# Optimization experiments

Measured on AMD Instinct MI355X. Metric: run time of the kernel, lower is better.

## Reference

```python
import jax, jax.numpy as jnp
import numpy as np

N = 6144      # nodes
DIN = 65      # input_dim (1 time + 64 space coords)
DOUT = 65     # output_dim per head
H = 4         # nheads
EPS = 1e-7
MIN = 1e-15
# curvature c = 1 throughout (MultiHeadGraphAttentionLayer hardcodes curvature=1)

def arcosh(z):
    return jnp.log(z + jnp.sqrt(jnp.maximum(z * z - 1.0, 0.0)))

def hyp_proj(u):
    # project onto hyperboloid: recompute time coord
    y = u[..., 1:]
    t = jnp.sqrt(1.0 + jnp.sum(y * y, -1, keepdims=True))
    return jnp.concatenate([t, y], -1)

def expmap0(u):
    v = u[..., 1:]
    n = jnp.maximum(jnp.linalg.norm(v, axis=-1, keepdims=True), MIN)
    return jnp.concatenate([jnp.cosh(n), jnp.sinh(n) * v / n], -1)

def logmap0(x):
    y = x[..., 1:]
    n = jnp.maximum(jnp.linalg.norm(y, axis=-1, keepdims=True), MIN)
    t = jnp.maximum(x[..., :1], 1.0 + EPS)
    return jnp.concatenate([jnp.zeros_like(t), arcosh(t) * y / n], -1)

def hyp_linear(x, W):
    # HypLinear (use_bias=False, eval mode): mobius_matvec = exp0(log0(x) @ W^T), then proj
    return hyp_proj(expmap0(logmap0(x) @ W.T))

def to_poincare(x):
    return x[..., 1:] / (x[..., :1] + 1.0)

def to_hyperboloid(p):
    s = jnp.sum(p * p, -1, keepdims=True)
    return jnp.concatenate([1.0 + s, 2.0 * p], -1) / jnp.maximum(1.0 - s, MIN)

def mobius_half(v):
    # 0.5 (x) v  (mobius scalar multiplication, c=1)
    n = jnp.maximum(jnp.linalg.norm(v, axis=-1, keepdims=True), MIN)
    return jnp.tanh(0.5 * jnp.arctanh(jnp.minimum(n, 1.0 - EPS))) * v / n

def head(x, adj_t, Wa, Wd, Wo):
    att = hyp_linear(x, Wa)   # [N, DOUT]
    red = hyp_linear(x, Wd)   # [N, DOUT]
    # pairwise hyperboloid sqdist via Minkowski inner product (negate time coord)
    am = att.at[:, 0].multiply(-1.0)
    theta = jnp.maximum(-(am @ att.T), 1.0 + EPS)          # [N, N]
    S = jnp.minimum(arcosh(theta) ** 2, 50.0)
    # coef[i, j] = -adj[j, i] * sqdist for incoming edges (mask = adj^T)
    coef = jnp.where(adj_t > 0.01, -adj_t * S, 0.0)
    # F.normalize along incoming-edge axis (zeros don't change the L2 norm)
    a = coef / jnp.maximum(jnp.linalg.norm(coef, axis=-1, keepdims=True), 1e-12)
    pv = to_poincare(red)                                   # [N, DOUT-1]
    lam = 2.0 / jnp.maximum(1.0 - jnp.sum(pv * pv, -1), MIN)  # conformal factors [N]
    num = (a * lam[None, :]) @ pv                           # [N, DOUT-1]
    den = jnp.sum(jnp.abs(a) * (lam - 1.0)[None, :], -1, keepdims=True)
    m = mobius_half(num / jnp.maximum(den, MIN))            # mobius midpoint
    return hyp_linear(to_hyperboloid(m), Wo)                # [N, DOUT]

def reference(x, adj, W_att, W_data, W_out, W_lin):
    adj_t = adj.T
    hs = jnp.stack([head(x, adj_t, W_att[h], W_data[h], W_out[h]) for h in range(H)], axis=1)  # [N, H, DOUT]
    p = to_poincare(hs).reshape(x.shape[0], -1)             # PoincareBall.concat -> [N, H*(DOUT-1)]
    return hyp_linear(to_hyperboloid(p), W_lin)             # [N, H*DOUT]

def setup_inputs():
    key = jax.random.key(0)
    ks = jax.random.split(key, 8)
    sp = 0.1 * jax.random.normal(ks[0], (N, DIN - 1), jnp.float32)
    x = jnp.concatenate([jnp.sqrt(1.0 + jnp.sum(sp * sp, -1, keepdims=True)), sp], -1)
    adj = (jax.random.uniform(ks[1], (N, N)) < 32.0 / N).astype(jnp.float32)
    adj = jnp.maximum(adj, jnp.eye(N, dtype=jnp.float32))  # every node >=1 incoming edge
    def xavier(k, shape):
        b = (6.0 / (shape[0] + shape[1])) ** 0.5
        return jax.random.uniform(k, shape, jnp.float32, -b, b)
    W_att = jnp.stack([xavier(jax.random.fold_in(ks[2], h), (DOUT, DIN)) for h in range(H)])
    W_data = jnp.stack([xavier(jax.random.fold_in(ks[3], h), (DOUT, DIN)) for h in range(H)])
    W_out = jnp.stack([xavier(jax.random.fold_in(ks[4], h), (DOUT, DOUT)) for h in range(H)])
    W_lin = xavier(ks[5], (H * DOUT, H * (DOUT - 1) + 1))
    return {"x": x, "adj": adj, "W_att": W_att, "W_data": W_data, "W_out": W_out, "W_lin": W_lin}
```

## Files before the change

kernel.cpp:

```cpp
#include <hip/hip_runtime.h>
#include <math.h>

#define N 6144
#define H 4
#define CAP 128
#define MINF 1e-15f
#define ONE_EPS  1.0000001192092896f
#define ONE_MEPS 0.9999998807907104f

__device__ __forceinline__ float wave_reduce_sum(float v) {
    v += __shfl_xor(v, 32, 64);
    v += __shfl_xor(v, 16, 64);
    v += __shfl_xor(v, 8, 64);
    v += __shfl_xor(v, 4, 64);
    v += __shfl_xor(v, 2, 64);
    v += __shfl_xor(v, 1, 64);
    return v;
}

__device__ __forceinline__ float arcosh_f(float z) {
    return logf(z + sqrtf(fmaxf(z * z - 1.0f, 0.0f)));
}

__global__ void k_prep(const float* __restrict__ x, float* __restrict__ lmv,
                       const float* __restrict__ W_att, const float* __restrict__ W_data,
                       const float* __restrict__ W_out, const float* __restrict__ Wl,
                       float* __restrict__ Bp, float* __restrict__ Bo,
                       float* __restrict__ WlT, int* __restrict__ cnt) {
    int b = blockIdx.x;
    if (b < 1536) {
        int i = b * 4 + (threadIdx.x >> 6);
        int lane = threadIdx.x & 63;
        float y = x[i * 65 + 1 + lane];
        float ss = wave_reduce_sum(y * y);
        float n = fmaxf(sqrtf(ss), MINF);
        float t = fmaxf(x[i * 65], ONE_EPS);
        lmv[i * 64 + lane] = arcosh_f(t) * y / n;
    } else if (b < 1728) {
        int tid = (b - 1536) * 256 + threadIdx.x;
        int m = tid >> 12;
        int r = tid & 4095;
        int k = r >> 6, o = r & 63;
        const float* src;
        if (m < 4) src = W_att + m * 65 * 65;
        else if (m < 8) src = W_data + (m - 4) * 65 * 65;
        else src = W_out + (m - 8) * 65 * 65;
        float val = src[(1 + o) * 65 + (1 + k)];
        if (m < 8) Bp[m * 4096 + k * 64 + o] = val;
        else Bo[(m - 8) * 4096 + k * 64 + o] = val;
    } else if (b < 1808) {
        int L = ((b - 1728) * 256 + threadIdx.x) * 4;
        int k = L / 320, o0 = L % 320;
        float v[4];
        #pragma unroll
        for (int q = 0; q < 4; q++) {
            int o = o0 + q;
            v[q] = (o < 259) ? Wl[(size_t)(1 + o) * 257 + 1 + k] : 0.f;
        }
        *(float4*)(WlT + L) = make_float4(v[0], v[1], v[2], v[3]);
    } else {
        cnt[(b - 1808) * 256 + threadIdx.x] = 0;
    }
}

__global__ void __launch_bounds__(256) k_csr_gemm(
        const float* __restrict__ adj, int* __restrict__ cnt, int* __restrict__ idx,
        const float* __restrict__ lmv, const float* __restrict__ Bp,
        float* __restrict__ attv, float2* __restrict__ a0l, float* __restrict__ pv) {
    __shared__ float smem[64 * 65];
    if (blockIdx.x < 768) {
        float (*As)[64] = (float(*)[64])smem;
        float (*Bs)[64] = (float(*)[64])(smem + 1024);
        float (*Cs)[65] = (float(*)[65])smem;
        int my = blockIdx.x / 96;
        int ix = blockIdx.x % 96;
        const float* Bb = Bp + (size_t)my * 4096;
        int i0 = ix * 64;
        int tid = threadIdx.x;
        int tx = tid & 15, ty = tid >> 4;
        float acc[4][4] = {};
        for (int k0 = 0; k0 < 64; k0 += 16) {
            {
                int mm = tid >> 2, kq = tid & 3;
                float4 v = *(const float4*)(lmv + (size_t)(i0 + mm) * 64 + k0 + kq * 4);
                As[kq * 4 + 0][mm] = v.x;
                As[kq * 4 + 1][mm] = v.y;
                As[kq * 4 + 2][mm] = v.z;
                As[kq * 4 + 3][mm] = v.w;
            }
            {
                int kk = tid >> 4, o4 = tid & 15;
                float4 bvv = *(const float4*)(Bb + (k0 + kk) * 64 + o4 * 4);
                *(float4*)&Bs[kk][o4 * 4] = bvv;
            }
            __syncthreads();
            #pragma unroll
            for (int kk = 0; kk < 16; kk++) {
                float4 av = *(const float4*)&As[kk][ty * 4];
                float4 bv = *(const float4*)&Bs[kk][tx * 4];
                float a[4] = {av.x, av.y, av.z, av.w};
                float b[4] = {bv.x, bv.y, bv.z, bv.w};
                #pragma unroll
                for (int r = 0; r < 4; r++)
                    #pragma unroll
                    for (int c = 0; c < 4; c++) acc[r][c] += a[r] * b[c];
            }
            __syncthreads();
        }
        #pragma unroll
        for (int r = 0; r < 4; r++)
            #pragma unroll
            for (int c = 0; c < 4; c++)
                Cs[ty * 4 + r][tx * 4 + c] = acc[r][c];
        __syncthreads();
        int w = tid >> 6, lane = tid & 63;
        bool isAtt = my < 4;
        int h = my & 3;
        #pragma unroll 1
        for (int r = 0; r < 16; r++) {
            int row = w * 16 + r;
            int i = i0 + row;
            float u = Cs[row][lane];
            float nn = fmaxf(sqrtf(wave_reduce_sum(u * u)), MINF);
            if (isAtt) {
                float sha = sinhf(nn);
                attv[((size_t)h * N + i) * 64 + lane] = sha * u / nn;
                if (lane == 0) a0l[h * N + i].x = coshf(nn);
            } else {
                float shd = sinhf(nn), chd = coshf(nn);
                float pvd = (shd * u / nn) / (chd + 1.0f);
                pv[((size_t)h * N + i) * 64 + lane] = pvd;
                float sp = wave_reduce_sum(pvd * pvd);
                if (lane == 0) a0l[h * N + i].y = 2.0f / fmaxf(1.0f - sp, MINF);
            }
        }
    } else {
        const float4* a4 = (const float4*)adj;
        const unsigned STRIDE = 1048576u;
        unsigned e0 = (blockIdx.x - 768) * 256 + threadIdx.x;
        float4 v0 = a4[e0];
        float4 v1 = a4[e0 + STRIDE];
        #pragma unroll 1
        for (int it = 0; it < 9; it++) {
            float4 vn;
            if (it < 7) vn = a4[e0 + (unsigned)(it + 2) * STRIDE];
            unsigned base = (e0 + (unsigned)it * STRIDE) * 4u;
            float vals[4] = {v0.x, v0.y, v0.z, v0.w};
            #pragma unroll
            for (int q = 0; q < 4; q++) {
                if (vals[q] > 0.01f) {
                    unsigned t = base + q;
                    int j = t / N;
                    int i = t % N;
                    int pos = atomicAdd(&cnt[i], 1);
                    if (pos < CAP) idx[i * CAP + pos] = j;
                }
            }
            v0 = v1;
            v1 = vn;
        }
    }
}

__global__ void __launch_bounds__(256) k_attn(
        const int* __restrict__ cnt, const int* __restrict__ idx,
        const float* __restrict__ attv, const float2* __restrict__ a0l,
        const float* __restrict__ pv, float* __restrict__ lm2) {
    __shared__ float wls[4][CAP];
    __shared__ int jls[4][CAP];
    int w = threadIdx.x >> 6, lane = threadIdx.x & 63;
    int i = blockIdx.x * 4 + w;
    int h = blockIdx.y;
    const float* attvh = attv + (size_t)h * N * 64;
    const float* pvh = pv + (size_t)h * N * 64;
    const float2* a0lh = a0l + (size_t)h * N;

    int c = lane & 3;
    float4 aireg[4];
    #pragma unroll
    for (int q = 0; q < 4; q++)
        aireg[q] = *(const float4*)(attvh + (size_t)i * 64 + q * 16 + c * 4);
    float ai0 = a0lh[i].x;
    int nn = min(cnt[i], CAP);

    float accd = 0.f, accss = 0.f;
    for (int base = 0; base < nn; base += 16) {
        int t = base + (lane >> 2);
        bool act = t < nn;
        int j = act ? idx[i * CAP + t] : i;
        float2 al = a0lh[j];
        float d = 0.f;
        #pragma unroll
        for (int q = 0; q < 4; q++) {
            float4 b = *(const float4*)(attvh + (size_t)j * 64 + q * 16 + c * 4);
            float4 a = aireg[q];
            d += a.x * b.x + a.y * b.y + a.z * b.z + a.w * b.w;
        }
        d += __shfl_xor(d, 1, 64);
        d += __shfl_xor(d, 2, 64);
        float theta = fmaxf(ai0 * al.x - d, ONE_EPS);
        float ar = arcosh_f(theta);
        float S = fminf(ar * ar, 50.0f);
        if (!act) S = 0.f;
        if (c == 0) {
            accd += S * (al.y - 1.0f);
            accss += S * S;
            wls[w][t] = S * al.y;
            jls[w][t] = j;
        }
    }
    accd = wave_reduce_sum(accd);
    accss = wave_reduce_sum(accss);
    float nrm = fmaxf(sqrtf(accss), 1e-12f);
    float den = fmaxf(accd / nrm, MINF);
    float scl = 1.0f / (nrm * den);

    float accn = 0.f;
    #pragma unroll 4
    for (int t = 0; t < nn; t++) {
        int j = jls[w][t];
        float wq = wls[w][t];
        accn = fmaf(wq, pvh[(size_t)j * 64 + lane], accn);
    }
    float v = -scl * accn;
    float nv = fmaxf(sqrtf(wave_reduce_sum(v * v)), MINF);
    float nc = fminf(nv, ONE_MEPS);
    float mh = tanhf(0.5f * atanhf(nc));
    float md = mh * v / nv;
    float s = wave_reduce_sum(md * md);
    float Dh = fmaxf(1.0f - s, MINF);
    float hb0 = (1.0f + s) / Dh;
    float hbv = 2.0f * md / Dh;
    float nh = fmaxf(2.0f * sqrtf(s) / Dh, MINF);
    float t2 = fmaxf(hb0, ONE_EPS);
    lm2[((size_t)h * N + i) * 64 + lane] = arcosh_f(t2) * hbv / nh;
}

__global__ void __launch_bounds__(256) k_gemm_out(
        const float* __restrict__ lm2, const float* __restrict__ Bo,
        float* __restrict__ p) {
    __shared__ float As[16][64];
    __shared__ float Bs[16][64];
    __shared__ float Cs[64][65];
    int h = blockIdx.y;
    const float* Ab = lm2 + (size_t)h * N * 64;
    const float* Bb = Bo + (size_t)h * 4096;
    int i0 = blockIdx.x * 64;
    int tid = threadIdx.x;
    int tx = tid & 15, ty = tid >> 4;
    float acc[4][4] = {};
    for (int k0 = 0; k0 < 64; k0 += 16) {
        {
            int mm = tid >> 2, kq = tid & 3;
            float4 v = *(const float4*)(Ab + (size_t)(i0 + mm) * 64 + k0 + kq * 4);
            As[kq * 4 + 0][mm] = v.x;
            As[kq * 4 + 1][mm] = v.y;
            As[kq * 4 + 2][mm] = v.z;
            As[kq * 4 + 3][mm] = v.w;
        }
        {
            int kk = tid >> 4, o4 = tid & 15;
            float4 bvv = *(const float4*)(Bb + (k0 + kk) * 64 + o4 * 4);
            *(float4*)&Bs[kk][o4 * 4] = bvv;
        }
        __syncthreads();
        #pragma unroll
        for (int kk = 0; kk < 16; kk++) {
            float4 av = *(const float4*)&As[kk][ty * 4];
            float4 bv = *(const float4*)&Bs[kk][tx * 4];
            float a[4] = {av.x, av.y, av.z, av.w};
            float b[4] = {bv.x, bv.y, bv.z, bv.w};
            #pragma unroll
            for (int r = 0; r < 4; r++)
                #pragma unroll
                for (int c = 0; c < 4; c++) acc[r][c] += a[r] * b[c];
        }
        __syncthreads();
    }
    #pragma unroll
    for (int r = 0; r < 4; r++)
        #pragma unroll
        for (int c = 0; c < 4; c++)
            Cs[ty * 4 + r][tx * 4 + c] = acc[r][c];
    __syncthreads();
    int w = tid >> 6, lane = tid & 63;
    #pragma unroll 1
    for (int r16 = 0; r16 < 16; r16++) {
        int row = w * 16 + r16;
        int i = i0 + row;
        float u = Cs[row][lane];
        float nv = fmaxf(sqrtf(wave_reduce_sum(u * u)), MINF);
        float sh = sinhf(nv), ch = coshf(nv);
        p[(size_t)i * 256 + h * 64 + lane] = (sh * u / nv) / (ch + 1.0f);
    }
}

__global__ void k_final_logmap(const float* __restrict__ p, float* __restrict__ lmF) {
    __shared__ float part[4];
    int i = blockIdx.x;
    int t = threadIdx.x;
    int w = t >> 6;
    float pd = p[(size_t)i * 256 + t];
    float ss = wave_reduce_sum(pd * pd);
    if ((t & 63) == 0) part[w] = ss;
    __syncthreads();
    float s = part[0] + part[1] + part[2] + part[3];
    float Dh = fmaxf(1.0f - s, MINF);
    float hb0 = (1.0f + s) / Dh;
    float hbv = 2.0f * pd / Dh;
    float n = fmaxf(2.0f * sqrtf(s) / Dh, MINF);
    float tt = fmaxf(hb0, ONE_EPS);
    lmF[(size_t)i * 256 + t] = arcosh_f(tt) * hbv / n;
}

__global__ void __launch_bounds__(256) k_final_gemm(
        const float* __restrict__ A, const float* __restrict__ WlT,
        float* __restrict__ U) {
    __shared__ float As[16][64];
    __shared__ float Bs[16][64];
    int i0 = blockIdx.x * 64;
    int o0 = blockIdx.y * 64;
    int tid = threadIdx.x;
    int tx = tid & 15, ty = tid >> 4;
    float acc[4][4] = {};
    for (int k0 = 0; k0 < 256; k0 += 16) {
        {
            int mm = tid >> 2;
            int kq = tid & 3;
            const float4 v = *(const float4*)(A + (size_t)(i0 + mm) * 256 + k0 + kq * 4);
            As[kq * 4 + 0][mm] = v.x;
            As[kq * 4 + 1][mm] = v.y;
            As[kq * 4 + 2][mm] = v.z;
            As[kq * 4 + 3][mm] = v.w;
        }
        {
            int kk = tid >> 4, o4 = tid & 15;
            *(float4*)&Bs[kk][o4 * 4] =
                *(const float4*)(WlT + (size_t)(k0 + kk) * 320 + o0 + o4 * 4);
        }
        __syncthreads();
        #pragma unroll
        for (int kk = 0; kk < 16; kk++) {
            float4 av = *(const float4*)&As[kk][ty * 4];
            float4 bv = *(const float4*)&Bs[kk][tx * 4];
            float a[4] = {av.x, av.y, av.z, av.w};
            float b[4] = {bv.x, bv.y, bv.z, bv.w};
            #pragma unroll
            for (int r = 0; r < 4; r++)
                #pragma unroll
                for (int c = 0; c < 4; c++) acc[r][c] += a[r] * b[c];
        }
        __syncthreads();
    }
    #pragma unroll
    for (int r = 0; r < 4; r++) {
        int i = i0 + ty * 4 + r;
        #pragma unroll
        for (int c = 0; c < 4; c++) {
            int o = o0 + tx * 4 + c;
            if (o < 259) U[(size_t)i * 260 + o] = acc[r][c];
        }
    }
}

__global__ void k_final_epilogue(const float* __restrict__ U, float* __restrict__ out) {
    __shared__ float part[4];
    int i = blockIdx.x;
    int t = threadIdx.x;
    float a = U[(size_t)i * 260 + t];
    float b = (t < 3) ? U[(size_t)i * 260 + 256 + t] : 0.f;
    float ss = wave_reduce_sum(a * a + b * b);
    if ((t & 63) == 0) part[t >> 6] = ss;
    __syncthreads();
    ss = part[0] + part[1] + part[2] + part[3];
    float nv = fmaxf(sqrtf(ss), MINF);
    float sh = sinhf(nv);
    float scale = sh / nv;
    out[(size_t)i * 260 + 1 + t] = scale * a;
    if (t < 3) out[(size_t)i * 260 + 257 + t] = scale * b;
    if (t == 0) out[(size_t)i * 260] = sqrtf(1.0f + sh * sh);
}

extern "C" void kernel_launch(void* const* d_in, const int* in_sizes, int n_in,
                              void* d_out, int out_size, void* d_ws, size_t ws_size,
                              hipStream_t stream) {
    const float* x = (const float*)d_in[0];
    const float* adj = (const float*)d_in[1];
    const float* W_att = (const float*)d_in[2];
    const float* W_data = (const float*)d_in[3];
    const float* W_out = (const float*)d_in[4];
    const float* W_lin = (const float*)d_in[5];
    float* out = (float*)d_out;

    char* ws = (char*)d_ws;
    size_t off = 0;
    auto alloc = [&](size_t bytes) {
        void* ptr = ws + off;
        off += (bytes + 255) & ~(size_t)255;
        return ptr;
    };
    int* cnt = (int*)alloc((size_t)N * 4);
    int* idx = (int*)alloc((size_t)N * CAP * 4);
    float* lmv = (float*)alloc((size_t)N * 64 * 4);
    float* attv = (float*)alloc((size_t)H * N * 64 * 4);
    float2* a0l = (float2*)alloc((size_t)H * N * 8);
    float* pvb = (float*)alloc((size_t)H * N * 64 * 4);
    float* lm2 = (float*)alloc((size_t)H * N * 64 * 4);
    float* Bp = (float*)alloc((size_t)8 * 4096 * 4);
    float* Bo = (float*)alloc((size_t)4 * 4096 * 4);
    float* WlT = (float*)alloc((size_t)256 * 320 * 4);
    float* U = (float*)alloc((size_t)N * 260 * 4);
    float* lmF = attv;
    float* p = pvb;

    k_prep<<<1832, 256, 0, stream>>>(x, lmv, W_att, W_data, W_out, W_lin,
                                     Bp, Bo, WlT, cnt);
    k_csr_gemm<<<4864, 256, 0, stream>>>(adj, cnt, idx, lmv, Bp, attv, a0l, pvb);
    k_attn<<<dim3(N / 4, H), 256, 0, stream>>>(cnt, idx, attv, a0l, pvb, lm2);
    k_gemm_out<<<dim3(N / 64, H), 256, 0, stream>>>(lm2, Bo, p);
    k_final_logmap<<<N, 256, 0, stream>>>(p, lmF);
    k_final_gemm<<<dim3(N / 64, 5), 256, 0, stream>>>(lmF, WlT, U);
    k_final_epilogue<<<N, 256, 0, stream>>>(U, out);
}
```

Before: 334.7 us.

## Fuse output GEMM, logmap, final GEMM and epilogue into one tail kernel

```diff
diff --git a/kernel.cpp b/kernel.cpp
--- a/kernel.cpp
+++ b/kernel.cpp
@@ -236,149 +236,146 @@
     lm2[((size_t)h * N + i) * 64 + lane] = arcosh_f(t2) * hbv / nh;
 }
 
-__global__ void __launch_bounds__(256) k_gemm_out(
+#define PS 272
+#define BS5 336
+__global__ void __launch_bounds__(256) k_tail(
         const float* __restrict__ lm2, const float* __restrict__ Bo,
-        float* __restrict__ p) {
-    __shared__ float As[16][64];
-    __shared__ float Bs[16][64];
-    __shared__ float Cs[64][65];
-    int h = blockIdx.y;
-    const float* Ab = lm2 + (size_t)h * N * 64;
-    const float* Bb = Bo + (size_t)h * 4096;
-    int i0 = blockIdx.x * 64;
+        const float* __restrict__ WlT, float* __restrict__ out) {
+    __shared__ float smem[5376 + 16 * PS];
+    float* As1 = smem;
+    float* Bs1 = smem + 1088;
+    float* Bs5 = smem;
+    float* P   = smem + 5376;
+
+    int i0 = blockIdx.x * 16;
     int tid = threadIdx.x;
-    int tx = tid & 15, ty = tid >> 4;
-    float acc[4][4] = {};
-    for (int k0 = 0; k0 < 64; k0 += 16) {
+    int ty = tid >> 4;
+    int tx = tid & 15;
+
+    for (int h = 0; h < H; h++) {
         {
-            int mm = tid >> 2, kq = tid & 3;
-            float4 v = *(const float4*)(Ab + (size_t)(i0 + mm) * 64 + k0 + kq * 4);
-            As[kq * 4 + 0][mm] = v.x;
-            As[kq * 4 + 1][mm] = v.y;
-            As[kq * 4 + 2][mm] = v.z;
-            As[kq * 4 + 3][mm] = v.w;
-        }
-        {
-            int kk = tid >> 4, o4 = tid & 15;
-            float4 bvv = *(const float4*)(Bb + (k0 + kk) * 64 + o4 * 4);
-            *(float4*)&Bs[kk][o4 * 4] = bvv;
-        }
-        __syncthreads();
-        #pragma unroll
-        for (int kk = 0; kk < 16; kk++) {
-            float4 av = *(const float4*)&As[kk][ty * 4];
-            float4 bv = *(const float4*)&Bs[kk][tx * 4];
-            float a[4] = {av.x, av.y, av.z, av.w};
-            float b[4] = {bv.x, bv.y, bv.z, bv.w};
-            #pragma unroll
-            for (int r = 0; r < 4; r++)
-                #pragma unroll
-                for (int c = 0; c < 4; c++) acc[r][c] += a[r] * b[c];
-        }
-        __syncthreads();
-    }
-    #pragma unroll
-    for (int r = 0; r < 4; r++)
-        #pragma unroll
-        for (int c = 0; c < 4; c++)
-            Cs[ty * 4 + r][tx * 4 + c] = acc[r][c];
+            float4 v = *(const float4*)(lm2 + ((size_t)h * N + i0 + ty) * 64 + tx * 4);
+            *(float4*)(As1 + ty * 68 + tx * 4) = v;
+        }
+        float acc[4] = {0.f, 0.f, 0.f, 0.f};
+        for (int k0 = 0; k0 < 64; k0 += 16) {
+            {
+                *(float4*)(Bs1 + ty * 64 + tx * 4) =
+                    *(const float4*)(Bo + (size_t)h * 4096 + (k0 + ty) * 64 + tx * 4);
+            }
+            __syncthreads();
+            #pragma unroll
+            for (int kk = 0; kk < 16; kk++) {
+                float a = As1[ty * 68 + k0 + kk];
+                float4 bv = *(const float4*)(Bs1 + kk * 64 + tx * 4);
+                acc[0] += a * bv.x;
+                acc[1] += a * bv.y;
+                acc[2] += a * bv.z;
+                acc[3] += a * bv.w;
+            }
+            __syncthreads();
+        }
+        float ss = acc[0] * acc[0] + acc[1] * acc[1] + acc[2] * acc[2] + acc[3] * acc[3];
+        ss += __shfl_xor(ss, 1, 64);
+        ss += __shfl_xor(ss, 2, 64);
+        ss += __shfl_xor(ss, 4, 64);
+        ss += __shfl_xor(ss, 8, 64);
+        float nn = fmaxf(sqrtf(ss), MINF);
+        float sh = sinhf(nn), ch = coshf(nn);
+        float* Pr = P + ty * PS + h * 64 + tx * 4;
+        Pr[0] = (sh * acc[0] / nn) / (ch + 1.0f);
+        Pr[1] = (sh * acc[1] / nn) / (ch + 1.0f);
+        Pr[2] = (sh * acc[2] / nn) / (ch + 1.0f);
+        Pr[3] = (sh * acc[3] / nn) / (ch + 1.0f);
+    }
     __syncthreads();
-    int w = tid >> 6, lane = tid & 63;
-    #pragma unroll 1
-    for (int r16 = 0; r16 < 16; r16++) {
-        int row = w * 16 + r16;
-        int i = i0 + row;
-        float u = Cs[row][lane];
-        float nv = fmaxf(sqrtf(wave_reduce_sum(u * u)), MINF);
-        float sh = sinhf(nv), ch = coshf(nv);
-        p[(size_t)i * 256 + h * 64 + lane] = (sh * u / nv) / (ch + 1.0f);
-    }
-}
-
-__global__ void k_final_logmap(const float* __restrict__ p, float* __restrict__ lmF) {
-    __shared__ float part[4];
-    int i = blockIdx.x;
-    int t = threadIdx.x;
-    int w = t >> 6;
-    float pd = p[(size_t)i * 256 + t];
-    float ss = wave_reduce_sum(pd * pd);
-    if ((t & 63) == 0) part[w] = ss;
+
+    {
+        float sp = 0.f;
+        float4 pl[4];
+        #pragma unroll
+        for (int q = 0; q < 4; q++) {
+            pl[q] = *(const float4*)(P + ty * PS + q * 64 + tx * 4);
+            sp += pl[q].x * pl[q].x + pl[q].y * pl[q].y
+                + pl[q].z * pl[q].z + pl[q].w * pl[q].w;
+        }
+        sp += __shfl_xor(sp, 1, 64);
+        sp += __shfl_xor(sp, 2, 64);
+        sp += __shfl_xor(sp, 4, 64);
+        sp += __shfl_xor(sp, 8, 64);
+        float Dh = fmaxf(1.0f - sp, MINF);
+        float t2 = fmaxf((1.0f + sp) / Dh, ONE_EPS);
+        float nh = fmaxf(2.0f * sqrtf(sp) / Dh, MINF);
+        float ar2 = arcosh_f(t2);
+        #pragma unroll
+        for (int q = 0; q < 4; q++) {
+            float4 v = pl[q];
+            v.x = ar2 * (2.0f * v.x / Dh) / nh;
+            v.y = ar2 * (2.0f * v.y / Dh) / nh;
+            v.z = ar2 * (2.0f * v.z / Dh) / nh;
+            v.w = ar2 * (2.0f * v.w / Dh) / nh;
+            *(float4*)(P + ty * PS + q * 64 + tx * 4) = v;
+        }
+    }
     __syncthreads();
-    float s = part[0] + part[1] + part[2] + part[3];
-    float Dh = fmaxf(1.0f - s, MINF);
-    float hb0 = (1.0f + s) / Dh;
-    float hbv = 2.0f * pd / Dh;
-    float n = fmaxf(2.0f * sqrtf(s) / Dh, MINF);
-    float tt = fmaxf(hb0, ONE_EPS);
-    lmF[(size_t)i * 256 + t] = arcosh_f(tt) * hbv / n;
-}
-
-__global__ void __launch_bounds__(256) k_final_gemm(
-        const float* __restrict__ A, const float* __restrict__ WlT,
-        float* __restrict__ U) {
-    __shared__ float As[16][64];
-    __shared__ float Bs[16][64];
-    int i0 = blockIdx.x * 64;
-    int o0 = blockIdx.y * 64;
-    int tid = threadIdx.x;
-    int tx = tid & 15, ty = tid >> 4;
-    float acc[4][4] = {};
+
+    float acc2[5][4] = {};
     for (int k0 = 0; k0 < 256; k0 += 16) {
         {
-            int mm = tid >> 2;
-            int kq = tid & 3;
-            const float4 v = *(const float4*)(A + (size_t)(i0 + mm) * 256 + k0 + kq * 4);
-            As[kq * 4 + 0][mm] = v.x;
-            As[kq * 4 + 1][mm] = v.y;
-            As[kq * 4 + 2][mm] = v.z;
-            As[kq * 4 + 3][mm] = v.w;
-        }
-        {
-            int kk = tid >> 4, o4 = tid & 15;
-            *(float4*)&Bs[kk][o4 * 4] =
-                *(const float4*)(WlT + (size_t)(k0 + kk) * 320 + o0 + o4 * 4);
+            #pragma unroll
+            for (int q = 0; q < 5; q++)
+                *(float4*)(Bs5 + ty * BS5 + q * 64 + tx * 4) =
+                    *(const float4*)(WlT + (size_t)(k0 + ty) * 320 + q * 64 + tx * 4);
         }
         __syncthreads();
         #pragma unroll
-        for (int kk = 0; kk < 16; kk++) {
-            float4 av = *(const float4*)&As[kk][ty * 4];
-            float4 bv = *(const float4*)&Bs[kk][tx * 4];
-            float a[4] = {av.x, av.y, av.z, av.w};
-            float b[4] = {bv.x, bv.y, bv.z, bv.w};
-            #pragma unroll
-            for (int r = 0; r < 4; r++)
+        for (int kq = 0; kq < 4; kq++) {
+            float4 pv4 = *(const float4*)(P + ty * PS + k0 + kq * 4);
+            float av[4] = {pv4.x, pv4.y, pv4.z, pv4.w};
+            #pragma unroll
+            for (int j = 0; j < 4; j++) {
+                float a = av[j];
+                int kk = kq * 4 + j;
                 #pragma unroll
-                for (int c = 0; c < 4; c++) acc[r][c] += a[r] * b[c];
+                for (int q = 0; q < 5; q++) {
+                    float4 bv = *(const float4*)(Bs5 + kk * BS5 + q * 64 + tx * 4);
+                    acc2[q][0] += a * bv.x;
+                    acc2[q][1] += a * bv.y;
+                    acc2[q][2] += a * bv.z;
+                    acc2[q][3] += a * bv.w;
+                }
+            }
         }
         __syncthreads();
     }
+
+    float ss2 = 0.f;
     #pragma unroll
-    for (int r = 0; r < 4; r++) {
-        int i = i0 + ty * 4 + r;
-        #pragma unroll
-        for (int c = 0; c < 4; c++) {
-            int o = o0 + tx * 4 + c;
-            if (o < 259) U[(size_t)i * 260 + o] = acc[r][c];
-        }
-    }
-}
-
-__global__ void k_final_epilogue(const float* __restrict__ U, float* __restrict__ out) {
-    __shared__ float part[4];
-    int i = blockIdx.x;
-    int t = threadIdx.x;
-    float a = U[(size_t)i * 260 + t];
-    float b = (t < 3) ? U[(size_t)i * 260 + 256 + t] : 0.f;
-    float ss = wave_reduce_sum(a * a + b * b);
-    if ((t & 63) == 0) part[t >> 6] = ss;
-    __syncthreads();
-    ss = part[0] + part[1] + part[2] + part[3];
-    float nv = fmaxf(sqrtf(ss), MINF);
-    float sh = sinhf(nv);
-    float scale = sh / nv;
-    out[(size_t)i * 260 + 1 + t] = scale * a;
-    if (t < 3) out[(size_t)i * 260 + 257 + t] = scale * b;
-    if (t == 0) out[(size_t)i * 260] = sqrtf(1.0f + sh * sh);
+    for (int q = 0; q < 5; q++)
+        ss2 += acc2[q][0] * acc2[q][0] + acc2[q][1] * acc2[q][1]
+             + acc2[q][2] * acc2[q][2] + acc2[q][3] * acc2[q][3];
+    ss2 += __shfl_xor(ss2, 1, 64);
+    ss2 += __shfl_xor(ss2, 2, 64);
+    ss2 += __shfl_xor(ss2, 4, 64);
+    ss2 += __shfl_xor(ss2, 8, 64);
+    float nv = fmaxf(sqrtf(ss2), MINF);
+    float sh2 = sinhf(nv);
+    float scale = sh2 / nv;
+    size_t ob = (size_t)(i0 + ty) * 260;
+    #pragma unroll
+    for (int q = 0; q < 4; q++) {
+        int o = q * 64 + tx * 4;
+        out[ob + 1 + o + 0] = scale * acc2[q][0];
+        out[ob + 1 + o + 1] = scale * acc2[q][1];
+        out[ob + 1 + o + 2] = scale * acc2[q][2];
+        out[ob + 1 + o + 3] = scale * acc2[q][3];
+    }
+    if (tx == 0) {
+        out[ob] = sqrtf(1.0f + sh2 * sh2);
+        out[ob + 257] = scale * acc2[4][0];
+        out[ob + 258] = scale * acc2[4][1];
+        out[ob + 259] = scale * acc2[4][2];
+    }
 }
 
 extern "C" void kernel_launch(void* const* d_in, const int* in_sizes, int n_in,
@@ -409,16 +406,10 @@
     float* Bp = (float*)alloc((size_t)8 * 4096 * 4);
     float* Bo = (float*)alloc((size_t)4 * 4096 * 4);
     float* WlT = (float*)alloc((size_t)256 * 320 * 4);
-    float* U = (float*)alloc((size_t)N * 260 * 4);
-    float* lmF = attv;
-    float* p = pvb;
 
     k_prep<<<1832, 256, 0, stream>>>(x, lmv, W_att, W_data, W_out, W_lin,
                                      Bp, Bo, WlT, cnt);
     k_csr_gemm<<<4864, 256, 0, stream>>>(adj, cnt, idx, lmv, Bp, attv, a0l, pvb);
     k_attn<<<dim3(N / 4, H), 256, 0, stream>>>(cnt, idx, attv, a0l, pvb, lm2);
-    k_gemm_out<<<dim3(N / 64, H), 256, 0, stream>>>(lm2, Bo, p);
-    k_final_logmap<<<N, 256, 0, stream>>>(p, lmF);
-    k_final_gemm<<<dim3(N / 64, 5), 256, 0, stream>>>(lmF, WlT, U);
-    k_final_epilogue<<<N, 256, 0, stream>>>(U, out);
-}
+    k_tail<<<N / 16, 256, 0, stream>>>(lm2, Bo, WlT, out);
+}
```

New measurement: 322.0 us. 3.8% less time.
